# Kernel tuning notes

Measured on AMD Instinct MI355X. Metric: run time of the kernel, lower is better.

## Reference

```python
import jax, jax.numpy as jnp
from jax import lax
import numpy as np

B, S, H, E = 512, 128, 512, 128
VEC_FEAT = 128
WORD_VOCABS = [1000, 500, 200]
GOAL_VOCAB = 32000
TACTIC_VOCAB = 1024
NUM_ENC_LAYERS = 3  # -> 2 extra encoder linear layers


def setup_inputs() -> dict:
    key = jax.random.key(0)
    ks = iter(jax.random.split(key, 32))
    s = 0.05
    inp = {}
    inp["vec_features"] = jax.random.normal(next(ks), (B, VEC_FEAT), dtype=jnp.float32)
    inp["word_features"] = jax.random.randint(next(ks), (B, len(WORD_VOCABS)), 0, 200)
    inp["goals"] = jax.random.randint(next(ks), (B, S), 0, GOAL_VOCAB)
    # word feature embedding tables (distinct vocab sizes)
    inp["wemb0"] = jax.random.normal(next(ks), (WORD_VOCABS[0], E), dtype=jnp.float32) * s
    inp["wemb1"] = jax.random.normal(next(ks), (WORD_VOCABS[1], E), dtype=jnp.float32) * s
    inp["wemb2"] = jax.random.normal(next(ks), (WORD_VOCABS[2], E), dtype=jnp.float32) * s
    # features_in: Linear(vec_feat + 3*E -> H), torch convention W [out, in]
    inp["feat_in_W"] = jax.random.normal(next(ks), (H, VEC_FEAT + len(WORD_VOCABS) * E), dtype=jnp.float32) * s
    inp["feat_in_b"] = jnp.zeros((H,), dtype=jnp.float32)
    # stacked encoder layers: (L-1) x Linear(H -> H)
    inp["enc_W"] = jax.random.normal(next(ks), (NUM_ENC_LAYERS - 1, H, H), dtype=jnp.float32) * s
    inp["enc_b"] = jnp.zeros((NUM_ENC_LAYERS - 1, H), dtype=jnp.float32)
    inp["goal_emb"] = jax.random.normal(next(ks), (GOAL_VOCAB, H), dtype=jnp.float32) * s
    # GRU weights, torch layout: [3H, H] with gate order (r, z, n)
    inp["gru_Wih"] = jax.random.normal(next(ks), (3 * H, H), dtype=jnp.float32) * s
    inp["gru_Whh"] = jax.random.normal(next(ks), (3 * H, H), dtype=jnp.float32) * s
    inp["gru_bih"] = jnp.zeros((3 * H,), dtype=jnp.float32)
    inp["gru_bhh"] = jnp.zeros((3 * H,), dtype=jnp.float32)
    inp["dec_in_W"] = jax.random.normal(next(ks), (H, 2 * H), dtype=jnp.float32) * s
    inp["dec_in_b"] = jnp.zeros((H,), dtype=jnp.float32)
    inp["dec_out_W"] = jax.random.normal(next(ks), (TACTIC_VOCAB, H), dtype=jnp.float32) * s
    inp["dec_out_b"] = jnp.zeros((TACTIC_VOCAB,), dtype=jnp.float32)
    return inp


def reference(vec_features, word_features, goals, wemb0, wemb1, wemb2,
              feat_in_W, feat_in_b, enc_W, enc_b, goal_emb,
              gru_Wih, gru_Whh, gru_bih, gru_bhh,
              dec_in_W, dec_in_b, dec_out_W, dec_out_b):
    batch = vec_features.shape[0]
    h = gru_Whh.shape[1]
    # Goal GRU branch: relu(embedding) per token, then GRU recurrence.
    x_seq = jax.nn.relu(goal_emb[goals])                    # [B, S, H]
    # Precompute input-side gate projections for all timesteps: [B, S, 3H]
    gi = jnp.einsum('bsh,gh->bsg', x_seq, gru_Wih) + gru_bih

    def step(hid, gi_t):
        gh = hid @ gru_Whh.T + gru_bhh                      # [B, 3H]
        i_r, i_z, i_n = jnp.split(gi_t, 3, axis=-1)
        h_r, h_z, h_n = jnp.split(gh, 3, axis=-1)
        r = jax.nn.sigmoid(i_r + h_r)
        z = jax.nn.sigmoid(i_z + h_z)
        n = jnp.tanh(i_n + r * h_n)
        new = (1.0 - z) * n + z * hid
        return new, None

    h0 = jnp.zeros((batch, h), dtype=x_seq.dtype)
    goal_data, _ = lax.scan(step, h0, jnp.swapaxes(gi, 0, 1))  # [B, H]

    # Features branch: word-feature embeddings + vec features -> MLP
    embs = [wemb0[word_features[:, 0]], wemb1[word_features[:, 1]], wemb2[word_features[:, 2]]]
    feats = jnp.concatenate([vec_features] + embs, axis=1)
    features_data = feats @ feat_in_W.T + feat_in_b
    for i in range(enc_W.shape[0]):
        features_data = jax.nn.relu(features_data) @ enc_W[i].T + enc_b[i]

    full = jax.nn.relu(jnp.concatenate([goal_data, features_data], axis=1))
    full = jax.nn.relu(full @ dec_in_W.T + dec_in_b)
    logits = full @ dec_out_W.T + dec_out_b
    return jax.nn.log_softmax(logits, axis=1)
```

## Files before the change

kernel.cpp:

```cpp
#include <hip/hip_runtime.h>
#include <hip/hip_bf16.h>

typedef unsigned short ushort_t;
typedef __attribute__((ext_vector_type(8))) short short8;
typedef __attribute__((ext_vector_type(4))) float f32x4;
typedef __attribute__((ext_vector_type(4))) int i32x4;

__device__ __forceinline__ ushort_t f2bf(float f) {
    unsigned x = __builtin_bit_cast(unsigned, f);
    unsigned r = x + 0x7fffu + ((x >> 16) & 1u);
    return (ushort_t)(r >> 16);
}
__device__ __forceinline__ float bf2f(ushort_t u) {
    return __builtin_bit_cast(float, ((unsigned)u) << 16);
}

__device__ __forceinline__ void store16_cc(void* p, i32x4 v) {
    asm volatile("global_store_dwordx4 %0, %1, off sc0 sc1" :: "v"(p), "v"(v) : "memory");
}
__device__ __forceinline__ i32x4 load16_cc(const void* p) {
    i32x4 r;
    asm volatile("global_load_dwordx4 %0, %1, off sc0 sc1" : "=v"(r) : "v"(p));
    return r;
}

template<bool RELU>
__global__ void k_conv(const float* __restrict__ src, ushort_t* __restrict__ dst, int n) {
    int i = (blockIdx.x * blockDim.x + threadIdx.x) * 4;
    int stride = gridDim.x * blockDim.x * 4;
    for (; i < n; i += stride) {
        float4 v = *(const float4*)(src + i);
        if (RELU) {
            v.x = fmaxf(v.x, 0.f); v.y = fmaxf(v.y, 0.f);
            v.z = fmaxf(v.z, 0.f); v.w = fmaxf(v.w, 0.f);
        }
        dst[i + 0] = f2bf(v.x); dst[i + 1] = f2bf(v.y);
        dst[i + 2] = f2bf(v.z); dst[i + 3] = f2bf(v.w);
    }
}

__global__ void k_whh_frag(const float* __restrict__ whh, ushort_t* __restrict__ out) {
    int idx = blockIdx.x * blockDim.x + threadIdx.x;
    if (idx >= 16 * 6 * 16 * 64 * 8) return;
    int e  = idx & 7;
    int s  = idx >> 3;
    int l  = s & 63;
    int s2 = s >> 6;
    int kk = s2 & 15;
    int s3 = s2 >> 4;
    int f  = s3 % 6;
    int j  = s3 / 6;
    int ng = (f >> 1) * 512 + j * 32 + (f & 1) * 16 + (l & 15);
    int k  = kk * 32 + ((l >> 4) << 3) + e;
    out[idx] = f2bf(whh[(size_t)ng * 512 + k]);
}

__global__ void k_feats(const float* __restrict__ vec, const int* __restrict__ wf,
                        const float* __restrict__ w0, const float* __restrict__ w1,
                        const float* __restrict__ w2, ushort_t* __restrict__ out) {
    int idx = blockIdx.x * blockDim.x + threadIdx.x;
    if (idx >= 512 * 512) return;
    int b = idx >> 9, k = idx & 511;
    float v;
    if (k < 128)       v = vec[b * 128 + k];
    else if (k < 256)  v = w0[wf[b * 3 + 0] * 128 + (k - 128)];
    else if (k < 384)  v = w1[wf[b * 3 + 1] * 128 + (k - 256)];
    else               v = w2[wf[b * 3 + 2] * 128 + (k - 384)];
    out[idx] = f2bf(v);
}

template<bool RELU, bool OUTBF>
__global__ __launch_bounds__(256) void k_gemm(const ushort_t* __restrict__ A,
                                              const ushort_t* __restrict__ W,
                                              const float* __restrict__ bias,
                                              void* __restrict__ Cout,
                                              int M, int N, int K) {
    __shared__ __attribute__((aligned(16))) ushort_t As[128 * 64];
    __shared__ __attribute__((aligned(16))) ushort_t Ws[128 * 64];
    const int tid = threadIdx.x;
    const int lane = tid & 63, w = tid >> 6;
    const int wm = w >> 1, wn = w & 1;
    const int m0 = blockIdx.y * 128, n0 = blockIdx.x * 128;
    const int l16 = lane & 15, lq = lane >> 4;
    f32x4 acc[4][4] = {};

    for (int k0 = 0; k0 < K; k0 += 64) {
        #pragma unroll
        for (int c = 0; c < 4; ++c) {
            int chunk = w * 4 + c;
            int d = chunk * 1024 + lane * 16;
            int row = d >> 7;
            int dlin = d ^ ((row & 7) << 4);
            int col = (dlin & 127) >> 1;
            const ushort_t* ga = A + (size_t)(m0 + row) * K + k0 + col;
            __builtin_amdgcn_global_load_lds(
                (const __attribute__((address_space(1))) void*)ga,
                (__attribute__((address_space(3))) void*)(((char*)As) + chunk * 1024),
                16, 0, 0);
        }
        #pragma unroll
        for (int c = 0; c < 4; ++c) {
            int chunk = w * 4 + c;
            int d = chunk * 1024 + lane * 16;
            int row = d >> 7;
            int dlin = d ^ ((row & 7) << 4);
            int col = (dlin & 127) >> 1;
            const ushort_t* gw = W + (size_t)(n0 + row) * K + k0 + col;
            __builtin_amdgcn_global_load_lds(
                (const __attribute__((address_space(1))) void*)gw,
                (__attribute__((address_space(3))) void*)(((char*)Ws) + chunk * 1024),
                16, 0, 0);
        }
        asm volatile("s_waitcnt vmcnt(0)" ::: "memory");
        __syncthreads();

        #pragma unroll
        for (int kk = 0; kk < 2; ++kk) {
            short8 af[4], bfr[4];
            #pragma unroll
            for (int m = 0; m < 4; ++m) {
                int row = wm * 64 + m * 16 + l16;
                int addr = (row * 128 + kk * 64 + lq * 16) ^ ((row & 7) << 4);
                af[m] = *(const short8*)((const char*)As + addr);
            }
            #pragma unroll
            for (int n = 0; n < 4; ++n) {
                int row = wn * 64 + n * 16 + l16;
                int addr = (row * 128 + kk * 64 + lq * 16) ^ ((row & 7) << 4);
                bfr[n] = *(const short8*)((const char*)Ws + addr);
            }
            #pragma unroll
            for (int m = 0; m < 4; ++m)
                #pragma unroll
                for (int n = 0; n < 4; ++n)
                    acc[m][n] = __builtin_amdgcn_mfma_f32_16x16x32_bf16(af[m], bfr[n], acc[m][n], 0, 0, 0);
        }
        __syncthreads();
    }

    #pragma unroll
    for (int m = 0; m < 4; ++m) {
        int row = m0 + wm * 64 + m * 16 + lq * 4;
        #pragma unroll
        for (int n = 0; n < 4; ++n) {
            int col = n0 + wn * 64 + n * 16 + l16;
            float bv = bias[col];
            #pragma unroll
            for (int r = 0; r < 4; ++r) {
                float v = acc[m][n][r] + bv;
                if (RELU) v = fmaxf(v, 0.f);
                if (OUTBF) ((ushort_t*)Cout)[(size_t)(row + r) * N + col] = f2bf(v);
                else       ((float*)Cout)[(size_t)(row + r) * N + col] = v;
            }
        }
    }
}

__global__ __launch_bounds__(128) void k_recur(const ushort_t* __restrict__ G,
                                               const ushort_t* __restrict__ WhhF,
                                               const int* __restrict__ goals,
                                               const float* __restrict__ bhh,
                                               ushort_t* __restrict__ Hx,
                                               int* __restrict__ flags,
                                               float* __restrict__ goal_out) {
    __shared__ __attribute__((aligned(16))) ushort_t Bs[6 * 16 * 64 * 8];
    __shared__ __attribute__((aligned(16))) ushort_t Hs[32 * 32];
    const int bid = blockIdx.x;
    const int rg = bid & 15;
    const int cg = bid >> 4;
    const int r0 = rg * 32, c0 = cg * 32;
    const int tid = threadIdx.x, lane = tid & 63, w = tid >> 6;
    const int l16 = lane & 15, lq = lane >> 4;

    {
        const ushort_t* src = WhhF + (size_t)cg * 49152;
        for (int c = 0; c < 48; ++c) {
            int chunk = w * 48 + c;
            const ushort_t* ga = src + chunk * 512 + lane * 8;
            __builtin_amdgcn_global_load_lds(
                (const __attribute__((address_space(1))) void*)ga,
                (__attribute__((address_space(3))) void*)(((char*)Bs) + chunk * 1024),
                16, 0, 0);
        }
        asm volatile("s_waitcnt vmcnt(0)" ::: "memory");
        __syncthreads();
    }

    const int rowbase = r0 + w * 16;
    float hst[2][4];
    #pragma unroll
    for (int q = 0; q < 2; ++q)
        #pragma unroll
        for (int r = 0; r < 4; ++r) hst[q][r] = 0.f;

    float bh[3][2];
    #pragma unroll
    for (int g = 0; g < 3; ++g)
        #pragma unroll
        for (int q = 0; q < 2; ++q) bh[g][q] = bhh[g * 512 + c0 + q * 16 + l16];

    for (int t = 0; t < 128; ++t) {
        float gir[4][2], giz[4][2], gin[4][2];
        #pragma unroll
        for (int r = 0; r < 4; ++r) {
            int brow = rowbase + lq * 4 + r;
            int tok = goals[brow * 128 + t];
            const ushort_t* gr = G + (size_t)tok * 1536;
            #pragma unroll
            for (int q = 0; q < 2; ++q) {
                int cl = c0 + q * 16 + l16;
                gir[r][q] = bf2f(gr[cl]);
                giz[r][q] = bf2f(gr[512 + cl]);
                gin[r][q] = bf2f(gr[1024 + cl]);
            }
        }

        f32x4 acc[6] = {};
        if (t) {
            const ushort_t* hb = Hx + ((size_t)(t & 1) << 18);
            short8 af[16];
            #pragma unroll
            for (int kk = 0; kk < 16; ++kk) {
                const ushort_t* pa = hb + (size_t)(rowbase + l16) * 512 + kk * 32 + lq * 8;
                af[kk] = __builtin_bit_cast(short8, load16_cc(pa));
            }
            asm volatile("s_waitcnt vmcnt(0)" ::: "memory");
            __builtin_amdgcn_sched_barrier(0);
            #pragma unroll
            for (int kk = 0; kk < 16; ++kk) {
                #pragma unroll
                for (int f = 0; f < 6; ++f) {
                    short8 bfr = *(const short8*)((const char*)Bs + ((f * 16 + kk) * 64 + lane) * 16);
                    acc[f] = __builtin_amdgcn_mfma_f32_16x16x32_bf16(af[kk], bfr, acc[f], 0, 0, 0);
                }
            }
        }

        #pragma unroll
        for (int r = 0; r < 4; ++r) {
            #pragma unroll
            for (int q = 0; q < 2; ++q) {
                float ir = gir[r][q], iz = giz[r][q], in_ = gin[r][q];
                float hr = acc[q][r] + bh[0][q];
                float hz = acc[2 + q][r] + bh[1][q];
                float hn = acc[4 + q][r] + bh[2][q];
                float rr = 1.f / (1.f + __expf(-(ir + hr)));
                float zz = 1.f / (1.f + __expf(-(iz + hz)));
                float x = in_ + rr * hn;
                float ax = fabsf(x);
                float th = 1.f - 2.f / (__expf(2.f * ax) + 1.f);
                th = copysignf(th, x);
                float hnew = (1.f - zz) * th + zz * hst[q][r];
                hst[q][r] = hnew;
                Hs[(w * 16 + lq * 4 + r) * 32 + q * 16 + l16] = f2bf(hnew);
            }
        }
        __syncthreads();

        {
            int row = tid >> 2, coff = (tid & 3) * 8;
            i32x4 v = *(const i32x4*)&Hs[row * 32 + coff];
            ushort_t* ho = Hx + ((size_t)((t + 1) & 1) << 18)
                         + (size_t)(r0 + row) * 512 + c0 + coff;
            store16_cc(ho, v);
        }
        asm volatile("s_waitcnt vmcnt(0)" ::: "memory");
        __syncthreads();

        if (tid == 0)
            __hip_atomic_store(&flags[bid], t + 1, __ATOMIC_RELAXED, __HIP_MEMORY_SCOPE_AGENT);
        if (tid < 16) {
            int* pf = &flags[(tid << 4) | rg];
            for (int it = 0; it < 100000; ++it) {
                if (__hip_atomic_load(pf, __ATOMIC_RELAXED, __HIP_MEMORY_SCOPE_AGENT) >= t + 1)
                    break;
                __builtin_amdgcn_s_sleep(1);
            }
        }
        __syncthreads();
    }

    #pragma unroll
    for (int r = 0; r < 4; ++r) {
        int brow = rowbase + lq * 4 + r;
        #pragma unroll
        for (int q = 0; q < 2; ++q) {
            int cl = c0 + q * 16 + l16;
            goal_out[(size_t)brow * 512 + cl] = hst[q][r];
        }
    }
}

__global__ void k_concat(const float* __restrict__ gd, const ushort_t* __restrict__ r2,
                         ushort_t* __restrict__ out) {
    int idx = blockIdx.x * blockDim.x + threadIdx.x;
    if (idx >= 512 * 1024) return;
    int b = idx >> 10, c = idx & 1023;
    out[idx] = (c < 512) ? f2bf(fmaxf(gd[b * 512 + c], 0.f)) : r2[b * 512 + (c - 512)];
}

__global__ __launch_bounds__(256) void k_lsm(float* __restrict__ logits) {
    __shared__ float sm[4];
    __shared__ float ss[4];
    float* p = logits + (size_t)blockIdx.x * 1024;
    int tid = threadIdx.x;
    float4 v = ((const float4*)p)[tid];
    float m = fmaxf(fmaxf(v.x, v.y), fmaxf(v.z, v.w));
    #pragma unroll
    for (int o = 32; o >= 1; o >>= 1) m = fmaxf(m, __shfl_xor(m, o));
    if ((tid & 63) == 0) sm[tid >> 6] = m;
    __syncthreads();
    m = fmaxf(fmaxf(sm[0], sm[1]), fmaxf(sm[2], sm[3]));
    float s = __expf(v.x - m) + __expf(v.y - m) + __expf(v.z - m) + __expf(v.w - m);
    #pragma unroll
    for (int o = 32; o >= 1; o >>= 1) s += __shfl_xor(s, o);
    if ((tid & 63) == 0) ss[tid >> 6] = s;
    __syncthreads();
    s = ss[0] + ss[1] + ss[2] + ss[3];
    float lse = m + logf(s);
    v.x -= lse; v.y -= lse; v.z -= lse; v.w -= lse;
    ((float4*)p)[tid] = v;
}

static constexpr size_t OFF_G     = 0;
static constexpr size_t OFF_AREL  = OFF_G     + 98304000ull;
static constexpr size_t OFF_WIH   = OFF_AREL  + 32768000ull;
static constexpr size_t OFF_WHHF  = OFF_WIH   + 1572864ull;
static constexpr size_t OFF_HX    = OFF_WHHF  + 1572864ull;
static constexpr size_t OFF_FLAGS = OFF_HX    + 1048576ull;
static constexpr size_t OFF_GOAL  = OFF_FLAGS + 1024ull;
static constexpr size_t OFF_FEATS = OFF_GOAL  + 1048576ull;
static constexpr size_t OFF_W0    = OFF_FEATS + 524288ull;
static constexpr size_t OFF_W12   = OFF_W0    + 524288ull;
static constexpr size_t OFF_R0    = OFF_W12   + 1048576ull;
static constexpr size_t OFF_R1    = OFF_R0    + 524288ull;
static constexpr size_t OFF_R2    = OFF_R1    + 524288ull;
static constexpr size_t OFF_DECA  = OFF_R2    + 524288ull;
static constexpr size_t OFF_WD1   = OFF_DECA  + 1048576ull;
static constexpr size_t OFF_D1    = OFF_WD1   + 1048576ull;
static constexpr size_t OFF_WD2   = OFF_D1    + 524288ull;
static constexpr size_t WS_NEED   = OFF_WD2   + 1048576ull;

extern "C" void kernel_launch(void* const* d_in, const int* in_sizes, int n_in,
                              void* d_out, int out_size, void* d_ws, size_t ws_size,
                              hipStream_t stream) {
    if (ws_size < WS_NEED) return;

    const float* vec   = (const float*)d_in[0];
    const int*   wf    = (const int*)d_in[1];
    const int*   goals = (const int*)d_in[2];
    const float* we0   = (const float*)d_in[3];
    const float* we1   = (const float*)d_in[4];
    const float* we2   = (const float*)d_in[5];
    const float* fiW   = (const float*)d_in[6];
    const float* fib   = (const float*)d_in[7];
    const float* encW  = (const float*)d_in[8];
    const float* encb  = (const float*)d_in[9];
    const float* gemb  = (const float*)d_in[10];
    const float* Wih   = (const float*)d_in[11];
    const float* Whh   = (const float*)d_in[12];
    const float* bih   = (const float*)d_in[13];
    const float* bhh   = (const float*)d_in[14];
    const float* diW   = (const float*)d_in[15];
    const float* dib   = (const float*)d_in[16];
    const float* doW   = (const float*)d_in[17];
    const float* dob   = (const float*)d_in[18];

    char* ws = (char*)d_ws;
    ushort_t* G_     = (ushort_t*)(ws + OFF_G);
    ushort_t* Arel   = (ushort_t*)(ws + OFF_AREL);
    ushort_t* WihB   = (ushort_t*)(ws + OFF_WIH);
    ushort_t* WhhF   = (ushort_t*)(ws + OFF_WHHF);
    ushort_t* Hx     = (ushort_t*)(ws + OFF_HX);
    int*      flags  = (int*)(ws + OFF_FLAGS);
    float*    goalD  = (float*)(ws + OFF_GOAL);
    ushort_t* featsA = (ushort_t*)(ws + OFF_FEATS);
    ushort_t* W0     = (ushort_t*)(ws + OFF_W0);
    ushort_t* W1     = (ushort_t*)(ws + OFF_W12);
    ushort_t* W2     = W1 + 262144;
    ushort_t* R0     = (ushort_t*)(ws + OFF_R0);
    ushort_t* R1     = (ushort_t*)(ws + OFF_R1);
    ushort_t* R2     = (ushort_t*)(ws + OFF_R2);
    ushort_t* DecA   = (ushort_t*)(ws + OFF_DECA);
    ushort_t* Wd1    = (ushort_t*)(ws + OFF_WD1);
    ushort_t* D1     = (ushort_t*)(ws + OFF_D1);
    ushort_t* Wd2    = (ushort_t*)(ws + OFF_WD2);

    hipMemsetAsync(ws + OFF_FLAGS, 0, 1024, stream);

    auto cgrid = [](int n) { int b = (n / 4 + 255) / 256; return b > 2048 ? 2048 : b; };
    k_conv<false><<<cgrid(786432),  256, 0, stream>>>(Wih,  WihB, 786432);
    k_conv<false><<<cgrid(262144),  256, 0, stream>>>(fiW,  W0,   262144);
    k_conv<false><<<cgrid(524288),  256, 0, stream>>>(encW, W1,   524288);
    k_conv<false><<<cgrid(524288),  256, 0, stream>>>(diW,  Wd1,  524288);
    k_conv<false><<<cgrid(524288),  256, 0, stream>>>(doW,  Wd2,  524288);
    k_conv<true ><<<2048,           256, 0, stream>>>(gemb, Arel, 16384000);
    k_whh_frag<<<3072, 256, 0, stream>>>(Whh, WhhF);
    k_feats<<<1024, 256, 0, stream>>>(vec, wf, we0, we1, we2, featsA);

    k_gemm<false, true><<<dim3(12, 250), 256, 0, stream>>>(Arel, WihB, bih, G_, 32000, 1536, 512);

    k_gemm<true, true><<<dim3(4, 4), 256, 0, stream>>>(featsA, W0, fib,        R0, 512, 512, 512);
    k_gemm<true, true><<<dim3(4, 4), 256, 0, stream>>>(R0,     W1, encb,       R1, 512, 512, 512);
    k_gemm<true, true><<<dim3(4, 4), 256, 0, stream>>>(R1,     W2, encb + 512, R2, 512, 512, 512);

    {
        const ushort_t* Gc = G_; const ushort_t* Wc = WhhF;
        const int* gc = goals; const float* bc = bhh;
        ushort_t* hx = Hx; int* fl = flags; float* go = goalD;
        void* kargs[] = { &Gc, &Wc, &gc, &bc, &hx, &fl, &go };
        hipLaunchCooperativeKernel((const void*)k_recur, dim3(256), dim3(128),
                                   kargs, 0, stream);
    }

    k_concat<<<2048, 256, 0, stream>>>(goalD, R2, DecA);
    k_gemm<true,  true ><<<dim3(4, 4), 256, 0, stream>>>(DecA, Wd1, dib, D1, 512, 512, 1024);
    k_gemm<false, false><<<dim3(8, 4), 256, 0, stream>>>(D1, Wd2, dob, (float*)d_out, 512, 1024, 512);
    k_lsm<<<512, 256, 0, stream>>>((float*)d_out);
}
```

Before: 1.211 ms.

## Prefetch next-step GRU input gates and stage goal tokens in LDS

The goal-token block for each workgroup is staged into LDS once at kernel start. The per-timestep gathered input-gate values for step t+1 are issued as raw loads during step t, overlapping the hidden-state MFMA work and the inter-block barrier. This takes the dependent token-then-gather global latency off the serial recurrence critical path. It costs more LDS and registers, and relies on a hand-counted vmcnt wait being correct.

After: 1.173 ms. -3.2%, faster.

```diff
diff --git a/kernel.cpp b/kernel.cpp
--- a/kernel.cpp
+++ b/kernel.cpp
@@ -21,6 +21,11 @@
 __device__ __forceinline__ i32x4 load16_cc(const void* p) {
     i32x4 r;
     asm volatile("global_load_dwordx4 %0, %1, off sc0 sc1" : "=v"(r) : "v"(p));
+    return r;
+}
+__device__ __forceinline__ unsigned load_u16_raw(const ushort_t* p) {
+    unsigned r;
+    asm volatile("global_load_ushort %0, %1, off" : "=v"(r) : "v"(p));
     return r;
 }
 
@@ -165,6 +170,7 @@
                                                float* __restrict__ goal_out) {
     __shared__ __attribute__((aligned(16))) ushort_t Bs[6 * 16 * 64 * 8];
     __shared__ __attribute__((aligned(16))) ushort_t Hs[32 * 32];
+    __shared__ __attribute__((aligned(16))) int Tk[32 * 128];
     const int bid = blockIdx.x;
     const int rg = bid & 15;
     const int cg = bid >> 4;
@@ -176,17 +182,25 @@
         const ushort_t* src = WhhF + (size_t)cg * 49152;
         for (int c = 0; c < 48; ++c) {
             int chunk = w * 48 + c;
-            const ushort_t* ga = src + chunk * 512 + lane * 8;
             __builtin_amdgcn_global_load_lds(
-                (const __attribute__((address_space(1))) void*)ga,
+                (const __attribute__((address_space(1))) void*)(src + chunk * 512 + lane * 8),
                 (__attribute__((address_space(3))) void*)(((char*)Bs) + chunk * 1024),
                 16, 0, 0);
         }
+        const int* tsrc = goals + r0 * 128;
+        for (int c = 0; c < 8; ++c) {
+            int chunk = w * 8 + c;
+            __builtin_amdgcn_global_load_lds(
+                (const __attribute__((address_space(1))) void*)(tsrc + chunk * 256 + lane * 4),
+                (__attribute__((address_space(3))) void*)(((char*)Tk) + chunk * 1024),
+                16, 0, 0);
+        }
         asm volatile("s_waitcnt vmcnt(0)" ::: "memory");
         __syncthreads();
     }
 
     const int rowbase = r0 + w * 16;
+    const int lrow = w * 16 + lq * 4;
     float hst[2][4];
     #pragma unroll
     for (int q = 0; q < 2; ++q)
@@ -199,22 +213,38 @@
         #pragma unroll
         for (int q = 0; q < 2; ++q) bh[g][q] = bhh[g * 512 + c0 + q * 16 + l16];
 
-    for (int t = 0; t < 128; ++t) {
-        float gir[4][2], giz[4][2], gin[4][2];
+    float gc[3][4][2];
+    #pragma unroll
+    for (int r = 0; r < 4; ++r) {
+        int tok = Tk[(lrow + r) * 128];
+        const ushort_t* gr = G + (size_t)tok * 1536;
+        #pragma unroll
+        for (int q = 0; q < 2; ++q) {
+            int cl = c0 + q * 16 + l16;
+            gc[0][r][q] = bf2f(gr[cl]);
+            gc[1][r][q] = bf2f(gr[512 + cl]);
+            gc[2][r][q] = bf2f(gr[1024 + cl]);
+        }
+    }
+
+    unsigned gn[3][4][2];
+    auto issueGN = [&](int tn) {
         #pragma unroll
         for (int r = 0; r < 4; ++r) {
-            int brow = rowbase + lq * 4 + r;
-            int tok = goals[brow * 128 + t];
+            int tok = Tk[(lrow + r) * 128 + tn];
             const ushort_t* gr = G + (size_t)tok * 1536;
             #pragma unroll
             for (int q = 0; q < 2; ++q) {
                 int cl = c0 + q * 16 + l16;
-                gir[r][q] = bf2f(gr[cl]);
-                giz[r][q] = bf2f(gr[512 + cl]);
-                gin[r][q] = bf2f(gr[1024 + cl]);
-            }
-        }
-
+                gn[0][r][q] = load_u16_raw(gr + cl);
+                gn[1][r][q] = load_u16_raw(gr + 512 + cl);
+                gn[2][r][q] = load_u16_raw(gr + 1024 + cl);
+            }
+        }
+    };
+
+    for (int t = 0; t < 128; ++t) {
+        const int tn = (t < 127) ? t + 1 : 127;
         f32x4 acc[6] = {};
         if (t) {
             const ushort_t* hb = Hx + ((size_t)(t & 1) << 18);
@@ -224,7 +254,8 @@
                 const ushort_t* pa = hb + (size_t)(rowbase + l16) * 512 + kk * 32 + lq * 8;
                 af[kk] = __builtin_bit_cast(short8, load16_cc(pa));
             }
-            asm volatile("s_waitcnt vmcnt(0)" ::: "memory");
+            issueGN(tn);
+            asm volatile("s_waitcnt vmcnt(24)" ::: "memory");
             __builtin_amdgcn_sched_barrier(0);
             #pragma unroll
             for (int kk = 0; kk < 16; ++kk) {
@@ -234,13 +265,15 @@
                     acc[f] = __builtin_amdgcn_mfma_f32_16x16x32_bf16(af[kk], bfr, acc[f], 0, 0, 0);
                 }
             }
+        } else {
+            issueGN(tn);
         }
 
         #pragma unroll
         for (int r = 0; r < 4; ++r) {
             #pragma unroll
             for (int q = 0; q < 2; ++q) {
-                float ir = gir[r][q], iz = giz[r][q], in_ = gin[r][q];
+                float ir = gc[0][r][q], iz = gc[1][r][q], in_ = gc[2][r][q];
                 float hr = acc[q][r] + bh[0][q];
                 float hz = acc[2 + q][r] + bh[1][q];
                 float hn = acc[4 + q][r] + bh[2][q];
@@ -265,6 +298,7 @@
             store16_cc(ho, v);
         }
         asm volatile("s_waitcnt vmcnt(0)" ::: "memory");
+        __builtin_amdgcn_sched_barrier(0);
         __syncthreads();
 
         if (tid == 0)
@@ -278,6 +312,14 @@
             }
         }
         __syncthreads();
+
+        #pragma unroll
+        for (int g = 0; g < 3; ++g)
+            #pragma unroll
+            for (int r = 0; r < 4; ++r)
+                #pragma unroll
+                for (int q = 0; q < 2; ++q)
+                    gc[g][r][q] = bf2f((ushort_t)gn[g][r][q]);
     }
 
     #pragma unroll
```
